# Kernel tuning notes

Hardware: AMD Instinct MI355X
Metric: run time of the kernel (lower is better)

The kernel has to match this reference:

```python
import jax, jax.numpy as jnp
import numpy as np

UNITS = 14336
IN_FEATURES = 4096
PACKED = IN_FEATURES // 4  # 4 ternary values (2 bits each) per byte
CLIP_VAL = 100.0

# 2-bit crumb -> ternary value lookup: 0 -> 0, 1 -> +1, 2 -> -1, 3 -> 0
_TERNARY_LUT = jnp.array([0.0, 1.0, -1.0, 0.0], dtype=jnp.float32)


def _unpack_ternary(pw):
    """pw: [U, P] int (byte values 0..255) -> dense ternary float W [U, 4*P].
    Little-endian crumbs within each byte (shifts 0,2,4,6)."""
    crumbs = jnp.stack([(pw >> (2 * i)) & 3 for i in range(4)], axis=-1)  # [U, P, 4]
    crumbs = crumbs.reshape(pw.shape[0], -1)  # [U, 4*P]
    return _TERNARY_LUT[crumbs][:, :IN_FEATURES]  # [U, IN]


def setup_inputs() -> dict:
    key = jax.random.key(0)
    k1, k2, k3, k4 = jax.random.split(key, 4)
    x = jax.random.normal(k1, (32, IN_FEATURES), dtype=jnp.float32)
    # packed ternary weights, one uint8-valued byte per 4 ternary weights
    pw = jax.random.randint(k2, (UNITS, PACKED), 0, 256, dtype=jnp.int32)
    scale = 1.0 + 0.02 * jax.random.normal(k3, (UNITS,), dtype=jnp.float32)
    bias = 0.01 * jax.random.normal(k4, (UNITS,), dtype=jnp.float32)
    return {"x": x, "pw": pw, "scale": scale, "bias": bias}


def reference(x, pw, scale, bias):
    # dense ternary weight [UNITS, IN]; kernel target would fuse this unpack into the GEMM
    W = _unpack_ternary(pw)
    y = jnp.einsum('bd,ud->bu', x, W)  # [B, UNITS]
    y = y * scale + bias               # per-unit affine dequant
    return jnp.clip(y, -CLIP_VAL, CLIP_VAL)
```

## Files before the change

### kernel.cpp

```cpp
#include <hip/hip_runtime.h>

#define UNITS 14336
#define IN_F 4096
#define PACKED 1024
#define CLIP_VAL 100.0f

typedef unsigned int uint32;

using bf16x8 = __attribute__((ext_vector_type(8))) short;
using f32x4  = __attribute__((ext_vector_type(4))) float;

__device__ inline unsigned short f2bf(float f) {
    uint32 u = __float_as_uint(f);
    u += 0x7FFFu + ((u >> 16) & 1u);
    return (unsigned short)(u >> 16);
}

__global__ __launch_bounds__(256) void convert_x_kernel(
    const float* __restrict__ x, uint4* __restrict__ ws) {
    int t = blockIdx.x * 256 + threadIdx.x;
    int s = t >> 7;
    int h = (t >> 6) & 1;
    int lane = t & 63;
    int b = h * 16 + (lane & 15);
    int k = s * 32 + ((lane >> 4) << 3);
    const float4* src = (const float4*)(x + b * IN_F + k);
    float4 lo = src[0];
    float4 hi = src[1];
    uint4 o;
    o.x = (uint32)f2bf(lo.x) | ((uint32)f2bf(lo.y) << 16);
    o.y = (uint32)f2bf(lo.z) | ((uint32)f2bf(lo.w) << 16);
    o.z = (uint32)f2bf(hi.x) | ((uint32)f2bf(hi.y) << 16);
    o.w = (uint32)f2bf(hi.z) | ((uint32)f2bf(hi.w) << 16);
    ws[t] = o;
}

__device__ inline void unpack_byte(int v, uint32& r0, uint32& r1) {
    uint32 t0 = ((uint32)v & 3u) | (((uint32)v & 0xCu) << 14);
    uint32 t1 = (((uint32)v >> 4) & 3u) | (((uint32)v & 0xC0u) << 10);
    uint32 s0 = t0 >> 1;
    uint32 s1 = t1 >> 1;
    uint32 nz0 = (t0 ^ s0) & 0x00010001u;
    uint32 nz1 = (t1 ^ s1) & 0x00010001u;
    r0 = nz0 * 0x3F80u + ((s0 & 0x00010001u) << 15);
    r1 = nz1 * 0x3F80u + ((s1 & 0x00010001u) << 15);
}

__device__ inline float clipf(float y) {
    return fminf(fmaxf(y, -CLIP_VAL), CLIP_VAL);
}

__global__ __launch_bounds__(512) void ternary_mm_kernel(
    const uint4* __restrict__ xw,
    const int*   __restrict__ pw,
    const float* __restrict__ scale,
    const float* __restrict__ bias,
    float*       __restrict__ out) {
    __shared__ f32x4 red[8][4][64];

    const int tid  = threadIdx.x;
    const int wid  = tid >> 6;
    const int lane = tid & 63;
    const int q    = lane >> 4;
    const int n    = lane & 15;
    const int u0   = blockIdx.x << 5;

    f32x4 acc00 = {0.f,0.f,0.f,0.f};
    f32x4 acc10 = {0.f,0.f,0.f,0.f};
    f32x4 acc01 = {0.f,0.f,0.f,0.f};
    f32x4 acc11 = {0.f,0.f,0.f,0.f};

    const int s_begin = wid << 4;
    const int* pA = pw + (size_t)(u0 + n)      * PACKED + (q << 1) + (s_begin << 3);
    const int* pB = pw + (size_t)(u0 + 16 + n) * PACKED + (q << 1) + (s_begin << 3);
    const uint4* xb = xw + (s_begin << 7) + lane;

    #pragma unroll 4
    for (int i = 0; i < 16; ++i) {
        uint4 a0u = xb[i * 128];
        uint4 a1u = xb[i * 128 + 64];
        int2 wA = *(const int2*)(pA + i * 8);
        int2 wB = *(const int2*)(pB + i * 8);

        uint4 bA, bB;
        unpack_byte(wA.x, bA.x, bA.y);
        unpack_byte(wA.y, bA.z, bA.w);
        unpack_byte(wB.x, bB.x, bB.y);
        unpack_byte(wB.y, bB.z, bB.w);
        bf16x8 fA = __builtin_bit_cast(bf16x8, bA);
        bf16x8 fB = __builtin_bit_cast(bf16x8, bB);
        bf16x8 x0 = __builtin_bit_cast(bf16x8, a0u);
        bf16x8 x1 = __builtin_bit_cast(bf16x8, a1u);

        acc00 = __builtin_amdgcn_mfma_f32_16x16x32_bf16(x0, fA, acc00, 0, 0, 0);
        acc10 = __builtin_amdgcn_mfma_f32_16x16x32_bf16(x1, fA, acc10, 0, 0, 0);
        acc01 = __builtin_amdgcn_mfma_f32_16x16x32_bf16(x0, fB, acc01, 0, 0, 0);
        acc11 = __builtin_amdgcn_mfma_f32_16x16x32_bf16(x1, fB, acc11, 0, 0, 0);
    }

    red[wid][0][lane] = acc00;
    red[wid][1][lane] = acc10;
    red[wid][2][lane] = acc01;
    red[wid][3][lane] = acc11;
    __syncthreads();

    if (tid < 256) {
        const int f = tid >> 6;
        const int l = tid & 63;
        f32x4 s = red[0][f][l];
        #pragma unroll
        for (int w = 1; w < 8; ++w) {
            f32x4 v = red[w][f][l];
            s[0] += v[0]; s[1] += v[1]; s[2] += v[2]; s[3] += v[3];
        }
        const int g = f >> 1;
        const int h = f & 1;
        const int u  = u0 + g * 16 + (l & 15);
        const int b0 = h * 16 + ((l >> 4) << 2);
        const float sc = scale[u];
        const float bi = bias[u];
        float* o = out + (size_t)b0 * UNITS + u;
        o[0 * UNITS] = clipf(s[0] * sc + bi);
        o[1 * UNITS] = clipf(s[1] * sc + bi);
        o[2 * UNITS] = clipf(s[2] * sc + bi);
        o[3 * UNITS] = clipf(s[3] * sc + bi);
    }
}

extern "C" void kernel_launch(void* const* d_in, const int* in_sizes, int n_in,
                              void* d_out, int out_size, void* d_ws, size_t ws_size,
                              hipStream_t stream) {
    const float* x     = (const float*)d_in[0];
    const int*   pw    = (const int*)d_in[1];
    const float* scale = (const float*)d_in[2];
    const float* bias  = (const float*)d_in[3];
    float* out = (float*)d_out;

    uint4* xw = (uint4*)d_ws;

    convert_x_kernel<<<64, 256, 0, stream>>>(x, xw);
    ternary_mm_kernel<<<UNITS / 32, 512, 0, stream>>>(xw, pw, scale, bias, out);
}
```

Before: 110.6 us.

## Fuse x bf16 conversion into ternary GEMM and widen per-iteration K chunk

Removes the separate convert_x kernel and converts fp32 activations to bf16 inside the GEMM loop, reading x directly from global memory. Each lane now loads 16 packed weight bytes (int4) and 16 floats per row per iteration, issuing 8 MFMAs per iteration over 8 iterations instead of 4 over 16. This saves a kernel launch and the workspace round trip. In exchange every block redoes the conversion and reads 4x larger fp32 x data, which is mostly served from cache.

```diff
diff --git a/kernel.cpp b/kernel.cpp
--- a/kernel.cpp
+++ b/kernel.cpp
@@ -16,23 +16,8 @@
     return (unsigned short)(u >> 16);
 }
 
-__global__ __launch_bounds__(256) void convert_x_kernel(
-    const float* __restrict__ x, uint4* __restrict__ ws) {
-    int t = blockIdx.x * 256 + threadIdx.x;
-    int s = t >> 7;
-    int h = (t >> 6) & 1;
-    int lane = t & 63;
-    int b = h * 16 + (lane & 15);
-    int k = s * 32 + ((lane >> 4) << 3);
-    const float4* src = (const float4*)(x + b * IN_F + k);
-    float4 lo = src[0];
-    float4 hi = src[1];
-    uint4 o;
-    o.x = (uint32)f2bf(lo.x) | ((uint32)f2bf(lo.y) << 16);
-    o.y = (uint32)f2bf(lo.z) | ((uint32)f2bf(lo.w) << 16);
-    o.z = (uint32)f2bf(hi.x) | ((uint32)f2bf(hi.y) << 16);
-    o.w = (uint32)f2bf(hi.z) | ((uint32)f2bf(hi.w) << 16);
-    ws[t] = o;
+__device__ inline uint32 pack2bf(float a, float b) {
+    return (uint32)f2bf(a) | ((uint32)f2bf(b) << 16);
 }
 
 __device__ inline void unpack_byte(int v, uint32& r0, uint32& r1) {
@@ -50,8 +35,8 @@
     return fminf(fmaxf(y, -CLIP_VAL), CLIP_VAL);
 }
 
-__global__ __launch_bounds__(512) void ternary_mm_kernel(
-    const uint4* __restrict__ xw,
+__global__ __launch_bounds__(512) void ternary_mm_fused_kernel(
+    const float* __restrict__ x,
     const int*   __restrict__ pw,
     const float* __restrict__ scale,
     const float* __restrict__ bias,
@@ -70,32 +55,58 @@
     f32x4 acc01 = {0.f,0.f,0.f,0.f};
     f32x4 acc11 = {0.f,0.f,0.f,0.f};
 
-    const int s_begin = wid << 4;
-    const int* pA = pw + (size_t)(u0 + n)      * PACKED + (q << 1) + (s_begin << 3);
-    const int* pB = pw + (size_t)(u0 + 16 + n) * PACKED + (q << 1) + (s_begin << 3);
-    const uint4* xb = xw + (s_begin << 7) + lane;
+    const int g0 = wid << 3;
+    const int* pA = pw + (size_t)(u0 + n)      * PACKED + (g0 << 4) + (q << 2);
+    const int* pB = pw + (size_t)(u0 + 16 + n) * PACKED + (g0 << 4) + (q << 2);
+    const float* x0 = x + (size_t)n        * IN_F + (g0 << 6) + (q << 4);
+    const float* x1 = x + (size_t)(16 + n) * IN_F + (g0 << 6) + (q << 4);
 
-    #pragma unroll 4
-    for (int i = 0; i < 16; ++i) {
-        uint4 a0u = xb[i * 128];
-        uint4 a1u = xb[i * 128 + 64];
-        int2 wA = *(const int2*)(pA + i * 8);
-        int2 wB = *(const int2*)(pB + i * 8);
+    #pragma unroll 2
+    for (int i = 0; i < 8; ++i) {
+        int4 wA = *(const int4*)(pA + (i << 4));
+        int4 wB = *(const int4*)(pB + (i << 4));
+        const float4* xa = (const float4*)(x0 + (i << 6));
+        const float4* xb = (const float4*)(x1 + (i << 6));
+        float4 a0 = xa[0], a1 = xa[1], a2 = xa[2], a3 = xa[3];
+        float4 b0 = xb[0], b1 = xb[1], b2 = xb[2], b3 = xb[3];
 
-        uint4 bA, bB;
-        unpack_byte(wA.x, bA.x, bA.y);
-        unpack_byte(wA.y, bA.z, bA.w);
-        unpack_byte(wB.x, bB.x, bB.y);
-        unpack_byte(wB.y, bB.z, bB.w);
-        bf16x8 fA = __builtin_bit_cast(bf16x8, bA);
-        bf16x8 fB = __builtin_bit_cast(bf16x8, bB);
-        bf16x8 x0 = __builtin_bit_cast(bf16x8, a0u);
-        bf16x8 x1 = __builtin_bit_cast(bf16x8, a1u);
+        uint4 fA_A, fA_B, fB_A, fB_B;
+        unpack_byte(wA.x, fA_A.x, fA_A.y);
+        unpack_byte(wA.y, fA_A.z, fA_A.w);
+        unpack_byte(wA.z, fA_B.x, fA_B.y);
+        unpack_byte(wA.w, fA_B.z, fA_B.w);
+        unpack_byte(wB.x, fB_A.x, fB_A.y);
+        unpack_byte(wB.y, fB_A.z, fB_A.w);
+        unpack_byte(wB.z, fB_B.x, fB_B.y);
+        unpack_byte(wB.w, fB_B.z, fB_B.w);
 
-        acc00 = __builtin_amdgcn_mfma_f32_16x16x32_bf16(x0, fA, acc00, 0, 0, 0);
-        acc10 = __builtin_amdgcn_mfma_f32_16x16x32_bf16(x1, fA, acc10, 0, 0, 0);
-        acc01 = __builtin_amdgcn_mfma_f32_16x16x32_bf16(x0, fB, acc01, 0, 0, 0);
-        acc11 = __builtin_amdgcn_mfma_f32_16x16x32_bf16(x1, fB, acc11, 0, 0, 0);
+        uint4 xh0A, xh0B, xh1A, xh1B;
+        xh0A.x = pack2bf(a0.x, a0.y); xh0A.y = pack2bf(a0.z, a0.w);
+        xh0A.z = pack2bf(a1.x, a1.y); xh0A.w = pack2bf(a1.z, a1.w);
+        xh0B.x = pack2bf(a2.x, a2.y); xh0B.y = pack2bf(a2.z, a2.w);
+        xh0B.z = pack2bf(a3.x, a3.y); xh0B.w = pack2bf(a3.z, a3.w);
+        xh1A.x = pack2bf(b0.x, b0.y); xh1A.y = pack2bf(b0.z, b0.w);
+        xh1A.z = pack2bf(b1.x, b1.y); xh1A.w = pack2bf(b1.z, b1.w);
+        xh1B.x = pack2bf(b2.x, b2.y); xh1B.y = pack2bf(b2.z, b2.w);
+        xh1B.z = pack2bf(b3.x, b3.y); xh1B.w = pack2bf(b3.z, b3.w);
+
+        bf16x8 vA_A = __builtin_bit_cast(bf16x8, fA_A);
+        bf16x8 vA_B = __builtin_bit_cast(bf16x8, fA_B);
+        bf16x8 vB_A = __builtin_bit_cast(bf16x8, fB_A);
+        bf16x8 vB_B = __builtin_bit_cast(bf16x8, fB_B);
+        bf16x8 v0A  = __builtin_bit_cast(bf16x8, xh0A);
+        bf16x8 v0B  = __builtin_bit_cast(bf16x8, xh0B);
+        bf16x8 v1A  = __builtin_bit_cast(bf16x8, xh1A);
+        bf16x8 v1B  = __builtin_bit_cast(bf16x8, xh1B);
+
+        acc00 = __builtin_amdgcn_mfma_f32_16x16x32_bf16(v0A, vA_A, acc00, 0, 0, 0);
+        acc10 = __builtin_amdgcn_mfma_f32_16x16x32_bf16(v1A, vA_A, acc10, 0, 0, 0);
+        acc01 = __builtin_amdgcn_mfma_f32_16x16x32_bf16(v0A, vB_A, acc01, 0, 0, 0);
+        acc11 = __builtin_amdgcn_mfma_f32_16x16x32_bf16(v1A, vB_A, acc11, 0, 0, 0);
+        acc00 = __builtin_amdgcn_mfma_f32_16x16x32_bf16(v0B, vA_B, acc00, 0, 0, 0);
+        acc10 = __builtin_amdgcn_mfma_f32_16x16x32_bf16(v1B, vA_B, acc10, 0, 0, 0);
+        acc01 = __builtin_amdgcn_mfma_f32_16x16x32_bf16(v0B, vB_B, acc01, 0, 0, 0);
+        acc11 = __builtin_amdgcn_mfma_f32_16x16x32_bf16(v1B, vB_B, acc11, 0, 0, 0);
     }
 
     red[wid][0][lane] = acc00;
@@ -135,9 +146,7 @@
     const float* scale = (const float*)d_in[2];
     const float* bias  = (const float*)d_in[3];
     float* out = (float*)d_out;
+    (void)d_ws; (void)ws_size;
 
-    uint4* xw = (uint4*)d_ws;
-
-    convert_x_kernel<<<64, 256, 0, stream>>>(x, xw);
-    ternary_mm_kernel<<<UNITS / 32, 512, 0, stream>>>(xw, pw, scale, bias, out);
+    ternary_mm_fused_kernel<<<UNITS / 32, 512, 0, stream>>>(x, pw, scale, bias, out);
 }
```

Measured after the change: 126.8 us. 1.15x slower.

## Halve units per block and widen per-lane weight loads to int4

Applied to the files above, without the earlier changes.

Each block now covers 16 units instead of 32, which doubles the grid to 896 blocks. Each lane loads 4 packed ints (16 bytes) per iteration instead of two 8-byte loads, and the x workspace is rearranged so the wider weight load matches the k ordering. The aim is better memory-level parallelism and CU occupancy on the weight stream, which dominates traffic. In exchange, each x fragment is reused across half as many units, so total x reads from cache double.

```diff
diff --git a/kernel.cpp b/kernel.cpp
--- a/kernel.cpp
+++ b/kernel.cpp
@@ -16,23 +16,8 @@
     return (unsigned short)(u >> 16);
 }
 
-__global__ __launch_bounds__(256) void convert_x_kernel(
-    const float* __restrict__ x, uint4* __restrict__ ws) {
-    int t = blockIdx.x * 256 + threadIdx.x;
-    int s = t >> 7;
-    int h = (t >> 6) & 1;
-    int lane = t & 63;
-    int b = h * 16 + (lane & 15);
-    int k = s * 32 + ((lane >> 4) << 3);
-    const float4* src = (const float4*)(x + b * IN_F + k);
-    float4 lo = src[0];
-    float4 hi = src[1];
-    uint4 o;
-    o.x = (uint32)f2bf(lo.x) | ((uint32)f2bf(lo.y) << 16);
-    o.y = (uint32)f2bf(lo.z) | ((uint32)f2bf(lo.w) << 16);
-    o.z = (uint32)f2bf(hi.x) | ((uint32)f2bf(hi.y) << 16);
-    o.w = (uint32)f2bf(hi.z) | ((uint32)f2bf(hi.w) << 16);
-    ws[t] = o;
+__device__ inline uint32 pack2bf(float a, float b) {
+    return (uint32)f2bf(a) | ((uint32)f2bf(b) << 16);
 }
 
 __device__ inline void unpack_byte(int v, uint32& r0, uint32& r1) {
@@ -50,72 +35,91 @@
     return fminf(fmaxf(y, -CLIP_VAL), CLIP_VAL);
 }
 
+
+__global__ __launch_bounds__(256) void convert_x_kernel(
+    const float* __restrict__ x, uint4* __restrict__ ws) {
+    int t = blockIdx.x * 256 + threadIdx.x;
+    int lane = t & 63;
+    int h = (t >> 6) & 1;
+    int s = (t >> 7) & 1;
+    int g = t >> 8;
+    int n = lane & 15;
+    int q = lane >> 4;
+    int b = h * 16 + n;
+    int k0 = g * 64 + q * 16 + s * 8;
+    const float4* src = (const float4*)(x + (size_t)b * IN_F + k0);
+    float4 lo = src[0];
+    float4 hi = src[1];
+    uint4 o;
+    o.x = pack2bf(lo.x, lo.y);
+    o.y = pack2bf(lo.z, lo.w);
+    o.z = pack2bf(hi.x, hi.y);
+    o.w = pack2bf(hi.z, hi.w);
+    ws[t] = o;
+}
+
 __global__ __launch_bounds__(512) void ternary_mm_kernel(
     const uint4* __restrict__ xw,
     const int*   __restrict__ pw,
     const float* __restrict__ scale,
     const float* __restrict__ bias,
     float*       __restrict__ out) {
-    __shared__ f32x4 red[8][4][64];
+    __shared__ f32x4 red[8][2][64];
 
     const int tid  = threadIdx.x;
     const int wid  = tid >> 6;
     const int lane = tid & 63;
     const int q    = lane >> 4;
     const int n    = lane & 15;
-    const int u0   = blockIdx.x << 5;
+    const int u0   = blockIdx.x << 4;
 
-    f32x4 acc00 = {0.f,0.f,0.f,0.f};
-    f32x4 acc10 = {0.f,0.f,0.f,0.f};
-    f32x4 acc01 = {0.f,0.f,0.f,0.f};
-    f32x4 acc11 = {0.f,0.f,0.f,0.f};
+    f32x4 acc0 = {0.f,0.f,0.f,0.f};
+    f32x4 acc1 = {0.f,0.f,0.f,0.f};
 
-    const int s_begin = wid << 4;
-    const int* pA = pw + (size_t)(u0 + n)      * PACKED + (q << 1) + (s_begin << 3);
-    const int* pB = pw + (size_t)(u0 + 16 + n) * PACKED + (q << 1) + (s_begin << 3);
-    const uint4* xb = xw + (s_begin << 7) + lane;
+    const int g0 = wid << 3;
+    const int*   pA = pw + (size_t)(u0 + n) * PACKED + (g0 << 4) + (q << 2);
+    const uint4* xb = xw + (g0 << 8) + lane;
 
     #pragma unroll 4
-    for (int i = 0; i < 16; ++i) {
-        uint4 a0u = xb[i * 128];
-        uint4 a1u = xb[i * 128 + 64];
-        int2 wA = *(const int2*)(pA + i * 8);
-        int2 wB = *(const int2*)(pB + i * 8);
+    for (int i = 0; i < 8; ++i) {
+        int4 w4 = *(const int4*)(pA + (i << 4));
+        uint4 x00 = xb[(i << 8)];
+        uint4 x01 = xb[(i << 8) + 64];
+        uint4 x10 = xb[(i << 8) + 128];
+        uint4 x11 = xb[(i << 8) + 192];
 
-        uint4 bA, bB;
-        unpack_byte(wA.x, bA.x, bA.y);
-        unpack_byte(wA.y, bA.z, bA.w);
-        unpack_byte(wB.x, bB.x, bB.y);
-        unpack_byte(wB.y, bB.z, bB.w);
-        bf16x8 fA = __builtin_bit_cast(bf16x8, bA);
-        bf16x8 fB = __builtin_bit_cast(bf16x8, bB);
-        bf16x8 x0 = __builtin_bit_cast(bf16x8, a0u);
-        bf16x8 x1 = __builtin_bit_cast(bf16x8, a1u);
+        uint4 fA, fB;
+        unpack_byte(w4.x, fA.x, fA.y);
+        unpack_byte(w4.y, fA.z, fA.w);
+        unpack_byte(w4.z, fB.x, fB.y);
+        unpack_byte(w4.w, fB.z, fB.w);
+        bf16x8 vA = __builtin_bit_cast(bf16x8, fA);
+        bf16x8 vB = __builtin_bit_cast(bf16x8, fB);
 
-        acc00 = __builtin_amdgcn_mfma_f32_16x16x32_bf16(x0, fA, acc00, 0, 0, 0);
-        acc10 = __builtin_amdgcn_mfma_f32_16x16x32_bf16(x1, fA, acc10, 0, 0, 0);
-        acc01 = __builtin_amdgcn_mfma_f32_16x16x32_bf16(x0, fB, acc01, 0, 0, 0);
-        acc11 = __builtin_amdgcn_mfma_f32_16x16x32_bf16(x1, fB, acc11, 0, 0, 0);
+        acc0 = __builtin_amdgcn_mfma_f32_16x16x32_bf16(
+            __builtin_bit_cast(bf16x8, x00), vA, acc0, 0, 0, 0);
+        acc1 = __builtin_amdgcn_mfma_f32_16x16x32_bf16(
+            __builtin_bit_cast(bf16x8, x01), vA, acc1, 0, 0, 0);
+        acc0 = __builtin_amdgcn_mfma_f32_16x16x32_bf16(
+            __builtin_bit_cast(bf16x8, x10), vB, acc0, 0, 0, 0);
+        acc1 = __builtin_amdgcn_mfma_f32_16x16x32_bf16(
+            __builtin_bit_cast(bf16x8, x11), vB, acc1, 0, 0, 0);
     }
 
-    red[wid][0][lane] = acc00;
-    red[wid][1][lane] = acc10;
-    red[wid][2][lane] = acc01;
-    red[wid][3][lane] = acc11;
+    red[wid][0][lane] = acc0;
+    red[wid][1][lane] = acc1;
     __syncthreads();
 
-    if (tid < 256) {
-        const int f = tid >> 6;
+    if (tid < 128) {
+        const int h = tid >> 6;
         const int l = tid & 63;
-        f32x4 s = red[0][f][l];
+        f32x4 s = red[0][h][l];
         #pragma unroll
         for (int w = 1; w < 8; ++w) {
-            f32x4 v = red[w][f][l];
+            f32x4 v = red[w][h][l];
             s[0] += v[0]; s[1] += v[1]; s[2] += v[2]; s[3] += v[3];
         }
-        const int g = f >> 1;
-        const int h = f & 1;
-        const int u  = u0 + g * 16 + (l & 15);
+        const int u  = u0 + (l & 15);
         const int b0 = h * 16 + ((l >> 4) << 2);
         const float sc = scale[u];
         const float bi = bias[u];
@@ -139,5 +143,5 @@
     uint4* xw = (uint4*)d_ws;
 
     convert_x_kernel<<<64, 256, 0, stream>>>(x, xw);
-    ternary_mm_kernel<<<UNITS / 32, 512, 0, stream>>>(xw, pw, scale, bias, out);
+    ternary_mm_kernel<<<UNITS / 16, 512, 0, stream>>>(xw, pw, scale, bias, out);
 }
```

Result: no change. 109.7 us (-0.8%).
